# Performance work log

Hardware: AMD Instinct MI355X
Metric: run time of the kernel (lower is better)

The kernel has to match this reference:

```python
import jax, jax.numpy as jnp
import numpy as np

DIM = 1024
STATE = 64
HEADS = 8
EXPAND = 2
INNER = DIM * EXPAND          # 2048
HEAD_DIM = INNER // HEADS     # 256
KERNEL = 4
B, L = 2, 2048
EPS = 1e-5


def setup_inputs() -> dict:
    key = jax.random.key(0)
    ks = jax.random.split(key, 12)
    s = 0.02
    return {
        "input_tensor": jax.random.normal(ks[0], (B, L, DIM), jnp.float32),
        "Wx": jax.random.normal(ks[1], (INNER, DIM), jnp.float32) * s,
        "Wz": jax.random.normal(ks[2], (INNER, DIM), jnp.float32) * s,
        "conv_w": jax.random.normal(ks[3], (INNER, 1, KERNEL), jnp.float32) * s,
        "conv_b": jnp.zeros((INNER,), jnp.float32),
        "Wb": jax.random.normal(ks[4], (HEADS * STATE, INNER), jnp.float32) * s,
        "Wc": jax.random.normal(ks[5], (HEADS * STATE, INNER), jnp.float32) * s,
        "Wdt": jax.random.normal(ks[6], (HEADS, INNER), jnp.float32) * s,
        "b_dt": jnp.zeros((HEADS,), jnp.float32),
        "log_a": jnp.log(jnp.full((HEADS,), 0.5, jnp.float32)),
        "d_param": jnp.ones((HEADS,), jnp.float32),
        "gn_w": jnp.ones((INNER,), jnp.float32),
        "gn_b": jnp.zeros((INNER,), jnp.float32),
        "Wout": jax.random.normal(ks[7], (DIM, INNER), jnp.float32) * s,
    }


def _causal_conv(x, conv_w, conv_b):
    # x: (B, L, INNER); depthwise conv, kernel 4, left-pad 3 (causal)
    x_pad = jnp.pad(x, ((0, 0), (KERNEL - 1, 0), (0, 0)))
    w = conv_w[:, 0, :]  # (INNER, K)
    y = sum(x_pad[:, k:k + x.shape[1], :] * w[:, k] for k in range(KERNEL))
    return y + conv_b


def _ssd_scan(x, b, c, dt, a):
    # x: (B,L,H,P) b,c: (B,L,H,N) dt: (B,L,H) a: (H,)
    state0 = jnp.zeros((x.shape[0], HEADS, STATE, HEAD_DIM), x.dtype)

    def step(state, inp):
        x_t, b_t, c_t, dt_t = inp  # (B,H,P),(B,H,N),(B,H,N),(B,H)
        decay = jnp.exp(dt_t * a)[..., None, None]          # (B,H,1,1)
        b_bar = (dt_t[..., None] * b_t)                      # (B,H,N)
        state = decay * state + b_bar[..., None] * x_t[:, :, None, :]
        y_t = jnp.einsum("bhn,bhnp->bhp", c_t, state)
        return state, y_t

    xs = (x.transpose(1, 0, 2, 3), b.transpose(1, 0, 2, 3),
          c.transpose(1, 0, 2, 3), dt.transpose(1, 0, 2))
    _, ys = jax.lax.scan(step, state0, xs)  # ys: (L,B,H,P)
    return ys.transpose(1, 0, 2, 3)


def reference(input_tensor, Wx, Wz, conv_w, conv_b, Wb, Wc, Wdt, b_dt,
              log_a, d_param, gn_w, gn_b, Wout):
    bsz, seq, _ = input_tensor.shape
    x = input_tensor @ Wx.T               # (B,L,INNER)
    z = input_tensor @ Wz.T
    x = _causal_conv(x, conv_w, conv_b)
    x = jax.nn.silu(x)
    b = (x @ Wb.T).reshape(bsz, seq, HEADS, STATE)
    c = (x @ Wc.T).reshape(bsz, seq, HEADS, STATE)
    dt = jax.nn.softplus(x @ Wdt.T + b_dt)  # (B,L,H)
    xh = x.reshape(bsz, seq, HEADS, HEAD_DIM)
    a = -jnp.exp(log_a)
    y = _ssd_scan(xh, b, c, dt, a)
    y = y + d_param[None, None, :, None] * xh
    # GroupNorm(HEADS, INNER) applied on (B, C, L): normalize per (batch, group)
    # over (channels-in-group, sequence)
    yg = y  # (B, L, H, P) -- groups are contiguous channel blocks = heads
    mean = yg.mean(axis=(1, 3), keepdims=True)
    var = yg.var(axis=(1, 3), keepdims=True)
    yn = (yg - mean) / jnp.sqrt(var + EPS)
    yn = yn * gn_w.reshape(1, 1, HEADS, HEAD_DIM) + gn_b.reshape(1, 1, HEADS, HEAD_DIM)
    yn = yn.reshape(bsz, seq, INNER)
    out = yn * jax.nn.silu(z)
    return out @ Wout.T
```

## Files before the change

### kernel.cpp

```cpp
#include <hip/hip_runtime.h>
#include <math.h>

#define DIM_   1024
#define STATE_ 64
#define HEADS_ 8
#define INNER_ 2048
#define HDIM_  256
#define B_     2
#define L_     2048
#define M_     (B_*L_)
#define EPS_   1e-5f
#define Q_     64
#define NC_    (L_/Q_)
#define NCHUNK_ (B_*HEADS_*NC_)
#define BCS_   1024
#define XZS_   4096

typedef _Float16 f16;
typedef __attribute__((ext_vector_type(8))) _Float16 half8;
typedef __attribute__((ext_vector_type(4))) _Float16 half4;
typedef __attribute__((ext_vector_type(4))) float    f32x4;

__device__ __forceinline__ float siluf(float x) { return x / (1.f + expf(-x)); }

__device__ __forceinline__ void gload_lds16(const void* g, void* l) {
    __builtin_amdgcn_global_load_lds((const __attribute__((address_space(1))) void*)g,
                                     (__attribute__((address_space(3))) void*)l, 16, 0, 0);
}

__global__ __launch_bounds__(256) void cast_all(const float* __restrict__ in0,
                                                const float* __restrict__ Wx,
                                                const float* __restrict__ Wz,
                                                const float* __restrict__ Wb,
                                                const float* __restrict__ Wc,
                                                const float* __restrict__ Wout,
                                                f16* __restrict__ input_h,
                                                f16* __restrict__ wxz_h,
                                                f16* __restrict__ wbc_h,
                                                f16* __restrict__ wout_h) {
    int i = blockIdx.x * 256 + threadIdx.x;
    const float* src; f16* dst; int off;
    if      (i < 1048576) { src = in0;  dst = input_h;            off = i; }
    else if (i < 1572864) { src = Wx;   dst = wxz_h;              off = i - 1048576; }
    else if (i < 2097152) { src = Wz;   dst = wxz_h + 2097152;    off = i - 1572864; }
    else if (i < 2359296) { src = Wb;   dst = wbc_h;              off = i - 2097152; }
    else if (i < 2621440) { src = Wc;   dst = wbc_h + 1048576;    off = i - 2359296; }
    else                  { src = Wout; dst = wout_h;             off = i - 2621440; }
    float4 v = *(const float4*)&src[(size_t)off * 4];
    half4 o;
    o[0] = (f16)v.x; o[1] = (f16)v.y; o[2] = (f16)v.z; o[3] = (f16)v.w;
    *(half4*)&dst[(size_t)off * 4] = o;
}

template<int BN, bool OUTF16, bool SILUZ>
__global__ __launch_bounds__(256) void hgemm(const f16* __restrict__ A,
                                             const f16* __restrict__ W,
                                             void* __restrict__ Cout,
                                             int K, int N) {
    constexpr int N_FR = BN / 32;
    constexpr int NITER = (128 + BN) / 64;
    __shared__ f16 sA[128 * 32];
    __shared__ f16 sW[BN * 32];
    const int tid  = threadIdx.x;
    const int wid  = tid >> 6;
    const int lane = tid & 63;

    const int nwg = gridDim.x * gridDim.y;
    const int id0 = blockIdx.y * gridDim.x + blockIdx.x;
    const int cpx = nwg >> 3;
    const int id  = (id0 & 7) * cpx + (id0 >> 3);
    const int gxsh = __ffs(gridDim.x) - 1;
    const int bm = (id >> gxsh) * 128;
    const int bn = (id & (gridDim.x - 1)) * BN;

    const int wr = wid >> 1, wc = wid & 1;
    const int r  = lane & 15, kg = lane >> 4;

    const f16* gsrc[NITER];
    f16* ldst[NITER];
#pragma unroll
    for (int i = 0; i < NITER; ++i) {
        int slot = tid + i * 256;
        if (slot < 512) {
            int row = slot >> 2;
            int kgv = ((slot & 3) ^ ((row >> 1) & 3)) * 8;
            gsrc[i] = A + (size_t)(bm + row) * K + kgv;
        } else {
            int row = (slot - 512) >> 2;
            int kgv = ((slot & 3) ^ ((row >> 1) & 3)) * 8;
            gsrc[i] = W + (size_t)(bn + row) * K + kgv;
        }
        int slot0 = (tid & ~63) + i * 256;
        ldst[i] = (slot0 < 512) ? &sA[slot0 * 8] : &sW[(slot0 - 512) * 8];
    }

    int aoff[4], boff[N_FR];
#pragma unroll
    for (int m = 0; m < 4; ++m) {
        int arow = wr * 64 + m * 16 + r;
        aoff[m] = arow * 32 + ((kg ^ ((arow >> 1) & 3)) << 3);
    }
#pragma unroll
    for (int n = 0; n < N_FR; ++n) {
        int wrow = wc * (BN / 2) + n * 16 + r;
        boff[n] = wrow * 32 + ((kg ^ ((wrow >> 1) & 3)) << 3);
    }

    f32x4 acc[4][N_FR];
#pragma unroll
    for (int m = 0; m < 4; ++m)
#pragma unroll
        for (int n = 0; n < N_FR; ++n) acc[m][n] = (f32x4)0.f;

    for (int k0 = 0; k0 < K; k0 += 32) {
#pragma unroll
        for (int i = 0; i < NITER; ++i) gload_lds16(gsrc[i] + k0, ldst[i]);
        __syncthreads();
        half8 av[4], bv[N_FR];
#pragma unroll
        for (int m = 0; m < 4; ++m) av[m] = *(const half8*)&sA[aoff[m]];
#pragma unroll
        for (int n = 0; n < N_FR; ++n) bv[n] = *(const half8*)&sW[boff[n]];
#pragma unroll
        for (int m = 0; m < 4; ++m)
#pragma unroll
            for (int n = 0; n < N_FR; ++n)
                acc[m][n] = __builtin_amdgcn_mfma_f32_16x16x32_f16(av[m], bv[n], acc[m][n], 0, 0, 0);
        __syncthreads();
    }

#pragma unroll
    for (int m = 0; m < 4; ++m)
#pragma unroll
        for (int n = 0; n < N_FR; ++n) {
            int row0o = bm + wr * 64 + m * 16 + kg * 4;
            int col   = bn + wc * (BN / 2) + n * 16 + r;
#pragma unroll
            for (int j = 0; j < 4; ++j) {
                float v = acc[m][n][j];
                if (SILUZ && col >= INNER_) v = siluf(v);
                if (OUTF16) ((f16*)Cout)[(size_t)(row0o + j) * N + col] = (f16)v;
                else        ((float*)Cout)[(size_t)(row0o + j) * N + col] = v;
            }
        }
}

__global__ __launch_bounds__(256) void conv_silu_dt(const f16* __restrict__ xz,
                                                    const float* __restrict__ cw,
                                                    const float* __restrict__ cb,
                                                    const float* __restrict__ Wdt,
                                                    const float* __restrict__ bdt,
                                                    f16* __restrict__ xc,
                                                    float* __restrict__ dtb) {
    __shared__ float sred[4][HEADS_];
    const int m = blockIdx.x;
    const int tid = threadIdx.x;
    const int c8 = tid * 8;
    const int t = m & (L_ - 1);
    float acc[8];
    float4 wv[8];
#pragma unroll
    for (int j = 0; j < 8; ++j) { acc[j] = cb[c8 + j]; wv[j] = *(const float4*)&cw[(c8 + j) * 4]; }
#pragma unroll
    for (int k = 0; k < 4; ++k) {
        int tt = t - 3 + k;
        if (tt >= 0) {
            half8 xv = *(const half8*)&xz[(size_t)(m - 3 + k) * XZS_ + c8];
#pragma unroll
            for (int j = 0; j < 8; ++j) acc[j] += (float)xv[j] * ((const float*)&wv[j])[k];
        }
    }
    float xf[8];
    half8 o;
#pragma unroll
    for (int j = 0; j < 8; ++j) { xf[j] = siluf(acc[j]); o[j] = (f16)xf[j]; }
    *(half8*)&xc[(size_t)m * INNER_ + c8] = o;

    float p[HEADS_];
#pragma unroll
    for (int h = 0; h < HEADS_; ++h) {
        float4 w0 = *(const float4*)&Wdt[h * INNER_ + c8];
        float4 w1 = *(const float4*)&Wdt[h * INNER_ + c8 + 4];
        p[h] = xf[0]*w0.x + xf[1]*w0.y + xf[2]*w0.z + xf[3]*w0.w
             + xf[4]*w1.x + xf[5]*w1.y + xf[6]*w1.z + xf[7]*w1.w;
    }
#pragma unroll
    for (int h = 0; h < HEADS_; ++h)
#pragma unroll
        for (int off = 32; off > 0; off >>= 1)
            p[h] += __shfl_down(p[h], off, 64);
    if ((tid & 63) == 0) {
#pragma unroll
        for (int h = 0; h < HEADS_; ++h) sred[tid >> 6][h] = p[h];
    }
    __syncthreads();
    if (tid < 32) {
        float v = sred[tid >> 3][tid & 7];
        v += __shfl_down(v, 16, 32);
        v += __shfl_down(v, 8, 32);
        if (tid < 8) {
            float s = v + bdt[tid];
            dtb[(size_t)m * HEADS_ + tid] = (s > 20.f) ? s : log1pf(expf(s));
        }
    }
}

__global__ __launch_bounds__(256) void xpose_k(const f16* __restrict__ xc,
                                               f16* __restrict__ xT,
                                               float* __restrict__ gstat) {
    __shared__ f16 sT[64][72];
    const int blk = blockIdx.x;
    const int bh = blk >> 7;
    const int rem = blk & 127;
    const int tt = rem >> 2;
    const int pt = rem & 3;
    const int b = bh >> 3, h = bh & 7;
    const int tid = threadIdx.x;
    if (blk == 0 && tid < 2 * B_ * HEADS_) gstat[tid] = 0.f;
#pragma unroll
    for (int it = 0; it < 2; ++it) {
        int q = tid + it * 256;
        int tr = q >> 3;
        int p0 = (q & 7) * 8;
        half8 v = *(const half8*)&xc[(size_t)(b * L_ + tt * 64 + tr) * INNER_ + h * HDIM_ + pt * 64 + p0];
        *(half8*)&sT[tr][p0] = v;
    }
    __syncthreads();
#pragma unroll
    for (int it = 0; it < 2; ++it) {
        int q = tid + it * 256;
        int pr = q >> 3;
        int t0 = (q & 7) * 8;
        half8 v;
#pragma unroll
        for (int j = 0; j < 8; ++j) v[j] = sT[t0 + j][pr];
        *(half8*)&xT[((size_t)bh * HDIM_ + pt * 64 + pr) * L_ + tt * 64 + t0] = v;
    }
}

__global__ __launch_bounds__(256) void ssd12(const f16* __restrict__ bc,
                                             const float* __restrict__ dtb,
                                             const float* __restrict__ log_a,
                                             const f16* __restrict__ xT,
                                             f16* __restrict__ pbuf,
                                             f16* __restrict__ sloc,
                                             float* __restrict__ eAbuf,
                                             float* __restrict__ cdecay) {
    __shared__ float sA[Q_], sDt[Q_], sw[Q_];
    __shared__ f16 sB[Q_ * Q_];
    const int tid = threadIdx.x;
    const int chunk = blockIdx.x;
    const int bh = chunk / NC_;
    const int ck = chunk - bh * NC_;
    const int b = bh >> 3, h = bh & 7;
    const int m0 = b * L_ + ck * Q_;

    const int s0 = tid >> 3,        n00 = (tid & 7) * 8;
    const int s1 = (tid + 256) >> 3, n01 = (tid & 7) * 8;
    half8 bv0 = *(const half8*)&bc[(size_t)(m0 + s0) * BCS_ + h * STATE_ + n00];
    half8 bv1 = *(const half8*)&bc[(size_t)(m0 + s1) * BCS_ + h * STATE_ + n01];

    if (tid < 64) {
        float dt = dtb[(size_t)(m0 + tid) * HEADS_ + h];
        float a = -expf(log_a[h]);
        float x = dt * a;
#pragma unroll
        for (int off = 1; off < 64; off <<= 1) {
            float v = __shfl_up(x, off, 64);
            if (tid >= off) x += v;
        }
        float Alast = __shfl(x, 63, 64);
        sA[tid] = x;
        sDt[tid] = dt;
        sw[tid] = expf(Alast - x) * dt;
        eAbuf[(size_t)(m0 + tid) * HEADS_ + h] = expf(x);
        if (tid == 0) cdecay[chunk] = expf(Alast);
    }
    __syncthreads();

    {
        float w0 = sw[s0], w1 = sw[s1];
        half8 o0, o1;
#pragma unroll
        for (int j = 0; j < 8; ++j) { o0[j] = (f16)((float)bv0[j] * w0); o1[j] = (f16)((float)bv1[j] * w1); }
        *(half8*)&sB[s0 * Q_ + (n00 ^ ((s0 & 7) << 3))] = o0;
        *(half8*)&sB[s1 * Q_ + (n01 ^ ((s1 & 7) << 3))] = o1;
    }

    const int w = tid >> 6, lane = tid & 63;
    const int r = lane & 15, kg = lane >> 4;

    {
        const int ft = w;
        const f16* Crow = bc + (size_t)(m0 + ft * 16 + r) * BCS_ + 512 + h * STATE_;
        half8 a0 = *(const half8*)(Crow + kg * 8);
        half8 a1 = *(const half8*)(Crow + 32 + kg * 8);
#pragma unroll
        for (int fs = 0; fs < 4; ++fs) {
            const f16* Brow = bc + (size_t)(m0 + fs * 16 + r) * BCS_ + h * STATE_;
            half8 b0 = *(const half8*)(Brow + kg * 8);
            half8 b1 = *(const half8*)(Brow + 32 + kg * 8);
            f32x4 g = (f32x4)0.f;
            g = __builtin_amdgcn_mfma_f32_16x16x32_f16(a0, b0, g, 0, 0, 0);
            g = __builtin_amdgcn_mfma_f32_16x16x32_f16(a1, b1, g, 0, 0, 0);
            int s = fs * 16 + r;
            float As = sA[s], dts = sDt[s];
#pragma unroll
            for (int j = 0; j < 4; ++j) {
                int t = ft * 16 + kg * 4 + j;
                float val = (t >= s) ? g[j] * expf(sA[t] - As) * dts : 0.f;
                pbuf[((size_t)chunk * Q_ + t) * Q_ + s] = (f16)val;
            }
        }
    }
    __syncthreads();

    f32x4 acc[4][4];
#pragma unroll
    for (int i = 0; i < 4; ++i)
#pragma unroll
        for (int j = 0; j < 4; ++j) acc[i][j] = (f32x4)0.f;

#pragma unroll
    for (int kk = 0; kk < 2; ++kk) {
        half8 a[4], bfr[4];
#pragma unroll
        for (int pf = 0; pf < 4; ++pf) {
            int p = w * 64 + pf * 16 + r;
            a[pf] = *(const half8*)&xT[((size_t)bh * HDIM_ + p) * L_ + ck * Q_ + kk * 32 + kg * 8];
        }
#pragma unroll
        for (int nf = 0; nf < 4; ++nf) {
            int n = nf * 16 + r;
            half8 v;
#pragma unroll
            for (int j = 0; j < 8; ++j) {
                int s = kk * 32 + kg * 8 + j;
                v[j] = sB[s * Q_ + (n ^ (j << 3))];
            }
            bfr[nf] = v;
        }
#pragma unroll
        for (int pf = 0; pf < 4; ++pf)
#pragma unroll
            for (int nf = 0; nf < 4; ++nf)
                acc[pf][nf] = __builtin_amdgcn_mfma_f32_16x16x32_f16(a[pf], bfr[nf], acc[pf][nf], 0, 0, 0);
    }
#pragma unroll
    for (int pf = 0; pf < 4; ++pf)
#pragma unroll
        for (int nf = 0; nf < 4; ++nf) {
            int n = nf * 16 + r;
#pragma unroll
            for (int j = 0; j < 4; ++j) {
                int p = w * 64 + pf * 16 + kg * 4 + j;
                sloc[((size_t)chunk * HDIM_ + p) * STATE_ + n] = (f16)acc[pf][nf][j];
            }
        }
}

__global__ __launch_bounds__(256) void chunk_scan_k(f16* __restrict__ sloc,
                                                    const float* __restrict__ cdecay) {
    int bh = blockIdx.x >> 4;
    int el4 = (((blockIdx.x & 15) * 256 + threadIdx.x) << 2);
    float s0 = 0.f, s1 = 0.f, s2 = 0.f, s3 = 0.f;
    for (int c = 0; c < NC_; ++c) {
        size_t chunk = (size_t)bh * NC_ + c;
        f16* ptr = sloc + chunk * (size_t)(STATE_ * HDIM_) + el4;
        half4 v = *(const half4*)ptr;
        half4 o; o[0] = (f16)s0; o[1] = (f16)s1; o[2] = (f16)s2; o[3] = (f16)s3;
        *(half4*)ptr = o;
        float d = cdecay[chunk];
        s0 = d * s0 + (float)v[0];
        s1 = d * s1 + (float)v[1];
        s2 = d * s2 + (float)v[2];
        s3 = d * s3 + (float)v[3];
    }
}

__global__ __launch_bounds__(256) void ssd_phase3(const f16* __restrict__ bc,
                                                  const f16* __restrict__ pbuf,
                                                  const f16* __restrict__ xT,
                                                  const f16* __restrict__ sloc,
                                                  const f16* __restrict__ xch,
                                                  const float* __restrict__ eAbuf,
                                                  const float* __restrict__ dparam,
                                                  f16* __restrict__ ybuf,
                                                  float* __restrict__ gstats) {
    __shared__ float red[512];
    const int tid = threadIdx.x;
    const int chunk = blockIdx.x;
    const int bh = chunk / NC_;
    const int ck = chunk - bh * NC_;
    const int b = bh >> 3, h = bh & 7;
    const int m0 = b * L_ + ck * Q_;
    const int w = tid >> 6, lane = tid & 63;
    const int r = lane & 15, kg = lane >> 4;

    float eA[4];
#pragma unroll
    for (int ft = 0; ft < 4; ++ft)
        eA[ft] = eAbuf[(size_t)(m0 + ft * 16 + r) * HEADS_ + h];

    f32x4 acc[4][4];
#pragma unroll
    for (int i = 0; i < 4; ++i)
#pragma unroll
        for (int j = 0; j < 4; ++j) acc[i][j] = (f32x4)0.f;

#pragma unroll
    for (int ks = 0; ks < 4; ++ks) {
        half8 a[4], bfr[4];
#pragma unroll
        for (int ft = 0; ft < 4; ++ft) {
            int t = ft * 16 + r;
            if (ks < 2) {
                a[ft] = *(const half8*)&pbuf[((size_t)chunk * Q_ + t) * Q_ + ks * 32 + kg * 8];
            } else {
                half8 c = *(const half8*)&bc[(size_t)(m0 + t) * BCS_ + 512 + h * STATE_ + (ks - 2) * 32 + kg * 8];
                half8 sc;
#pragma unroll
                for (int j = 0; j < 8; ++j) sc[j] = (f16)(eA[ft] * (float)c[j]);
                a[ft] = sc;
            }
        }
#pragma unroll
        for (int pf = 0; pf < 4; ++pf) {
            int p = w * 64 + pf * 16 + r;
            if (ks < 2)
                bfr[pf] = *(const half8*)&xT[((size_t)bh * HDIM_ + p) * L_ + ck * Q_ + ks * 32 + kg * 8];
            else
                bfr[pf] = *(const half8*)&sloc[((size_t)chunk * HDIM_ + p) * STATE_ + (ks - 2) * 32 + kg * 8];
        }
#pragma unroll
        for (int ft = 0; ft < 4; ++ft)
#pragma unroll
            for (int pf = 0; pf < 4; ++pf)
                acc[ft][pf] = __builtin_amdgcn_mfma_f32_16x16x32_f16(a[ft], bfr[pf], acc[ft][pf], 0, 0, 0);
    }

    const float d = dparam[h];
    float lsum = 0.f, lsq = 0.f;
#pragma unroll
    for (int ft = 0; ft < 4; ++ft)
#pragma unroll
        for (int pf = 0; pf < 4; ++pf) {
            int p = w * 64 + pf * 16 + r;
#pragma unroll
            for (int j = 0; j < 4; ++j) {
                int t = ft * 16 + kg * 4 + j;
                size_t off = (size_t)(m0 + t) * INNER_ + h * HDIM_ + p;
                float y = acc[ft][pf][j] + d * (float)xch[off];
                ybuf[off] = (f16)y;
                lsum += y; lsq += y * y;
            }
        }
    __syncthreads();
    red[tid] = lsum; red[256 + tid] = lsq;
    __syncthreads();
    for (int st = 128; st > 0; st >>= 1) {
        if (tid < st) { red[tid] += red[tid + st]; red[256 + tid] += red[256 + tid + st]; }
        __syncthreads();
    }
    if (tid == 0) {
        atomicAdd(&gstats[bh * 2 + 0], red[0]);
        atomicAdd(&gstats[bh * 2 + 1], red[256]);
    }
}

__global__ __launch_bounds__(256) void gn_gate_h(const f16* __restrict__ ybuf,
                                                 const f16* __restrict__ xz,
                                                 const float* __restrict__ gstats,
                                                 const float* __restrict__ gnw,
                                                 const float* __restrict__ gnb,
                                                 f16* __restrict__ g) {
    int idx = blockIdx.x * 256 + threadIdx.x;
    int c8 = (idx & (INNER_/8 - 1)) * 8;
    int m = idx >> 8;
    int bh = (m >> 11) * HEADS_ + (c8 >> 8);
    const float cnt = (float)(L_ * HDIM_);
    float mean = gstats[bh*2] / cnt;
    float var  = gstats[bh*2+1] / cnt - mean*mean;
    float rstd = rsqrtf(var + EPS_);
    size_t off = (size_t)m * INNER_ + c8;
    half8 yv = *(const half8*)&ybuf[off];
    half8 zv = *(const half8*)&xz[(size_t)m * XZS_ + INNER_ + c8];
    float4 w0 = *(const float4*)&gnw[c8], w1 = *(const float4*)&gnw[c8+4];
    float4 b0 = *(const float4*)&gnb[c8], b1 = *(const float4*)&gnb[c8+4];
    float wv[8] = {w0.x, w0.y, w0.z, w0.w, w1.x, w1.y, w1.z, w1.w};
    float bv[8] = {b0.x, b0.y, b0.z, b0.w, b1.x, b1.y, b1.z, b1.w};
    half8 o;
#pragma unroll
    for (int j = 0; j < 8; ++j) {
        float v = ((float)yv[j] - mean) * rstd * wv[j] + bv[j];
        o[j] = (f16)(v * (float)zv[j]);
    }
    *(half8*)&g[off] = o;
}

extern "C" void kernel_launch(void* const* d_in, const int* in_sizes, int n_in,
                              void* d_out, int out_size, void* d_ws, size_t ws_size,
                              hipStream_t stream) {
    const float* input  = (const float*)d_in[0];
    const float* Wx     = (const float*)d_in[1];
    const float* Wz     = (const float*)d_in[2];
    const float* conv_w = (const float*)d_in[3];
    const float* conv_b = (const float*)d_in[4];
    const float* Wb     = (const float*)d_in[5];
    const float* Wc     = (const float*)d_in[6];
    const float* Wdt    = (const float*)d_in[7];
    const float* b_dt   = (const float*)d_in[8];
    const float* log_a  = (const float*)d_in[9];
    const float* d_par  = (const float*)d_in[10];
    const float* gn_w   = (const float*)d_in[11];
    const float* gn_b   = (const float*)d_in[12];
    const float* Wout   = (const float*)d_in[13];
    float* out = (float*)d_out;

    float* ws = (float*)d_ws;
    size_t off = 0;
    auto alloc = [&](size_t nfloats) { float* p = ws + off; off += (nfloats + 63) & ~(size_t)63; return p; };
    f16* input_h = (f16*)alloc((size_t)M_*DIM_/2);
    f16* wxz_h   = (f16*)alloc((size_t)XZS_*DIM_/2);
    f16* wbc_h   = (f16*)alloc((size_t)BCS_*INNER_/2);
    f16* wout_h  = (f16*)alloc((size_t)DIM_*INNER_/2);
    f16* xz_h    = (f16*)alloc((size_t)M_*XZS_/2);
    f16* xconv_h = (f16*)alloc((size_t)M_*INNER_/2);
    f16* xT_h    = (f16*)alloc((size_t)M_*INNER_/2);
    f16* gbuf_h  = (f16*)alloc((size_t)M_*INNER_/2);
    f16* bcmat_h = (f16*)alloc((size_t)M_*BCS_/2);
    f16* pbuf_h  = (f16*)alloc((size_t)NCHUNK_*Q_*Q_/2);
    f16* sloc_h  = (f16*)alloc((size_t)NCHUNK_*STATE_*HDIM_/2);
    f16* ybuf_h  = (f16*)alloc((size_t)M_*INNER_/2);
    float* dtb   = alloc((size_t)M_*HEADS_);
    float* eAb   = alloc((size_t)M_*HEADS_);
    float* cdec  = alloc((size_t)NCHUNK_);
    float* gstat = alloc((size_t)2*B_*HEADS_);

    dim3 blk(256);

    cast_all<<<12288, blk, 0, stream>>>(input, Wx, Wz, Wb, Wc, Wout,
                                        input_h, wxz_h, wbc_h, wout_h);
    hgemm<128,true,true><<<dim3(XZS_/128, M_/128), blk, 0, stream>>>(input_h, wxz_h, xz_h, DIM_, XZS_);
    conv_silu_dt<<<M_, blk, 0, stream>>>(xz_h, conv_w, conv_b, Wdt, b_dt, xconv_h, dtb);
    hgemm<64,true,false><<<dim3(BCS_/64, M_/128), blk, 0, stream>>>(xconv_h, wbc_h, bcmat_h, INNER_, BCS_);
    xpose_k<<<2048, blk, 0, stream>>>(xconv_h, xT_h, gstat);
    ssd12<<<NCHUNK_, blk, 0, stream>>>(bcmat_h, dtb, log_a, xT_h, pbuf_h, sloc_h, eAb, cdec);
    chunk_scan_k<<<256, blk, 0, stream>>>(sloc_h, cdec);
    ssd_phase3<<<NCHUNK_, blk, 0, stream>>>(bcmat_h, pbuf_h, xT_h, sloc_h, xconv_h,
                                            eAb, d_par, ybuf_h, gstat);
    gn_gate_h<<<(M_*(INNER_/8))/256, blk, 0, stream>>>(ybuf_h, xz_h, gstat, gn_w, gn_b, gbuf_h);
    hgemm<64,false,false><<<dim3(DIM_/64, M_/128), blk, 0, stream>>>(gbuf_h, wout_h, out, INNER_, DIM_);
}
```

Baseline: 363.2 us.

## Double GEMM K-tile to 64, drop tile swizzle, fold D skip into diagonal

The shared fp16 GEMM now stages a K-step of 64 per iteration with an 8-way XOR swizzle, which halves the number of barrier pairs per output tile at the cost of twice the LDS footprint. The grouped workgroup-ID remapping for L2 locality is removed in favour of plain block indexing. The D·x skip term is folded into the intra-chunk diagonal of the P matrix in ssd12, so phase 3 no longer re-reads the conv output. Adding d to the diagonal in fp16 may slightly change numerics.

```diff
diff --git a/kernel.cpp b/kernel.cpp
--- a/kernel.cpp
+++ b/kernel.cpp
@@ -58,21 +58,14 @@
                                              void* __restrict__ Cout,
                                              int K, int N) {
     constexpr int N_FR = BN / 32;
-    constexpr int NITER = (128 + BN) / 64;
-    __shared__ f16 sA[128 * 32];
-    __shared__ f16 sW[BN * 32];
+    constexpr int NITER = (128 + BN) / 32;
+    __shared__ f16 sA[128 * 64];
+    __shared__ f16 sW[BN * 64];
     const int tid  = threadIdx.x;
     const int wid  = tid >> 6;
     const int lane = tid & 63;
-
-    const int nwg = gridDim.x * gridDim.y;
-    const int id0 = blockIdx.y * gridDim.x + blockIdx.x;
-    const int cpx = nwg >> 3;
-    const int id  = (id0 & 7) * cpx + (id0 >> 3);
-    const int gxsh = __ffs(gridDim.x) - 1;
-    const int bm = (id >> gxsh) * 128;
-    const int bn = (id & (gridDim.x - 1)) * BN;
-
+    const int bm = blockIdx.y * 128;
+    const int bn = blockIdx.x * BN;
     const int wr = wid >> 1, wc = wid & 1;
     const int r  = lane & 15, kg = lane >> 4;
 
@@ -81,29 +74,29 @@
 #pragma unroll
     for (int i = 0; i < NITER; ++i) {
         int slot = tid + i * 256;
-        if (slot < 512) {
-            int row = slot >> 2;
-            int kgv = ((slot & 3) ^ ((row >> 1) & 3)) * 8;
-            gsrc[i] = A + (size_t)(bm + row) * K + kgv;
+        if (slot < 1024) {
+            int row = slot >> 3;
+            int col = ((slot & 7) ^ (row & 7)) * 8;
+            gsrc[i] = A + (size_t)(bm + row) * K + col;
         } else {
-            int row = (slot - 512) >> 2;
-            int kgv = ((slot & 3) ^ ((row >> 1) & 3)) * 8;
-            gsrc[i] = W + (size_t)(bn + row) * K + kgv;
+            int row = (slot - 1024) >> 3;
+            int col = ((slot & 7) ^ (row & 7)) * 8;
+            gsrc[i] = W + (size_t)(bn + row) * K + col;
         }
         int slot0 = (tid & ~63) + i * 256;
-        ldst[i] = (slot0 < 512) ? &sA[slot0 * 8] : &sW[(slot0 - 512) * 8];
-    }
-
-    int aoff[4], boff[N_FR];
+        ldst[i] = (slot0 < 1024) ? &sA[slot0 * 8] : &sW[(slot0 - 1024) * 8];
+    }
+
+    int abase[4], axor[4], bbase[N_FR], bxor[N_FR];
 #pragma unroll
     for (int m = 0; m < 4; ++m) {
         int arow = wr * 64 + m * 16 + r;
-        aoff[m] = arow * 32 + ((kg ^ ((arow >> 1) & 3)) << 3);
+        abase[m] = arow * 64; axor[m] = arow & 7;
     }
 #pragma unroll
     for (int n = 0; n < N_FR; ++n) {
         int wrow = wc * (BN / 2) + n * 16 + r;
-        boff[n] = wrow * 32 + ((kg ^ ((wrow >> 1) & 3)) << 3);
+        bbase[n] = wrow * 64; bxor[n] = wrow & 7;
     }
 
     f32x4 acc[4][N_FR];
@@ -112,20 +105,25 @@
 #pragma unroll
         for (int n = 0; n < N_FR; ++n) acc[m][n] = (f32x4)0.f;
 
-    for (int k0 = 0; k0 < K; k0 += 32) {
+    for (int k0 = 0; k0 < K; k0 += 64) {
 #pragma unroll
         for (int i = 0; i < NITER; ++i) gload_lds16(gsrc[i] + k0, ldst[i]);
         __syncthreads();
-        half8 av[4], bv[N_FR];
-#pragma unroll
-        for (int m = 0; m < 4; ++m) av[m] = *(const half8*)&sA[aoff[m]];
-#pragma unroll
-        for (int n = 0; n < N_FR; ++n) bv[n] = *(const half8*)&sW[boff[n]];
-#pragma unroll
-        for (int m = 0; m < 4; ++m)
+#pragma unroll
+        for (int kk = 0; kk < 2; ++kk) {
+            half8 av[4], bv[N_FR];
+#pragma unroll
+            for (int m = 0; m < 4; ++m)
+                av[m] = *(const half8*)&sA[abase[m] + ((((kk << 2) | kg)) ^ axor[m]) * 8];
 #pragma unroll
             for (int n = 0; n < N_FR; ++n)
-                acc[m][n] = __builtin_amdgcn_mfma_f32_16x16x32_f16(av[m], bv[n], acc[m][n], 0, 0, 0);
+                bv[n] = *(const half8*)&sW[bbase[n] + ((((kk << 2) | kg)) ^ bxor[n]) * 8];
+#pragma unroll
+            for (int m = 0; m < 4; ++m)
+#pragma unroll
+                for (int n = 0; n < N_FR; ++n)
+                    acc[m][n] = __builtin_amdgcn_mfma_f32_16x16x32_f16(av[m], bv[n], acc[m][n], 0, 0, 0);
+        }
         __syncthreads();
     }
 
@@ -241,6 +239,7 @@
 __global__ __launch_bounds__(256) void ssd12(const f16* __restrict__ bc,
                                              const float* __restrict__ dtb,
                                              const float* __restrict__ log_a,
+                                             const float* __restrict__ dparam,
                                              const f16* __restrict__ xT,
                                              f16* __restrict__ pbuf,
                                              f16* __restrict__ sloc,
@@ -291,6 +290,7 @@
     const int r = lane & 15, kg = lane >> 4;
 
     {
+        const float dpar = dparam[h];
         const int ft = w;
         const f16* Crow = bc + (size_t)(m0 + ft * 16 + r) * BCS_ + 512 + h * STATE_;
         half8 a0 = *(const half8*)(Crow + kg * 8);
@@ -309,6 +309,7 @@
             for (int j = 0; j < 4; ++j) {
                 int t = ft * 16 + kg * 4 + j;
                 float val = (t >= s) ? g[j] * expf(sA[t] - As) * dts : 0.f;
+                if (t == s) val += dpar;
                 pbuf[((size_t)chunk * Q_ + t) * Q_ + s] = (f16)val;
             }
         }
@@ -382,11 +383,10 @@
                                                   const f16* __restrict__ pbuf,
                                                   const f16* __restrict__ xT,
                                                   const f16* __restrict__ sloc,
-                                                  const f16* __restrict__ xch,
                                                   const float* __restrict__ eAbuf,
-                                                  const float* __restrict__ dparam,
-                                                  f16* __restrict__ ybuf,
+                                                  float* __restrict__ ybuf16_,
                                                   float* __restrict__ gstats) {
+    f16* ybuf = (f16*)ybuf16_;
     __shared__ float red[512];
     const int tid = threadIdx.x;
     const int chunk = blockIdx.x;
@@ -439,7 +439,6 @@
                 acc[ft][pf] = __builtin_amdgcn_mfma_f32_16x16x32_f16(a[ft], bfr[pf], acc[ft][pf], 0, 0, 0);
     }
 
-    const float d = dparam[h];
     float lsum = 0.f, lsq = 0.f;
 #pragma unroll
     for (int ft = 0; ft < 4; ++ft)
@@ -450,7 +449,7 @@
             for (int j = 0; j < 4; ++j) {
                 int t = ft * 16 + kg * 4 + j;
                 size_t off = (size_t)(m0 + t) * INNER_ + h * HDIM_ + p;
-                float y = acc[ft][pf][j] + d * (float)xch[off];
+                float y = acc[ft][pf][j];
                 ybuf[off] = (f16)y;
                 lsum += y; lsq += y * y;
             }
@@ -545,10 +544,10 @@
     conv_silu_dt<<<M_, blk, 0, stream>>>(xz_h, conv_w, conv_b, Wdt, b_dt, xconv_h, dtb);
     hgemm<64,true,false><<<dim3(BCS_/64, M_/128), blk, 0, stream>>>(xconv_h, wbc_h, bcmat_h, INNER_, BCS_);
     xpose_k<<<2048, blk, 0, stream>>>(xconv_h, xT_h, gstat);
-    ssd12<<<NCHUNK_, blk, 0, stream>>>(bcmat_h, dtb, log_a, xT_h, pbuf_h, sloc_h, eAb, cdec);
+    ssd12<<<NCHUNK_, blk, 0, stream>>>(bcmat_h, dtb, log_a, d_par, xT_h, pbuf_h, sloc_h, eAb, cdec);
     chunk_scan_k<<<256, blk, 0, stream>>>(sloc_h, cdec);
-    ssd_phase3<<<NCHUNK_, blk, 0, stream>>>(bcmat_h, pbuf_h, xT_h, sloc_h, xconv_h,
-                                            eAb, d_par, ybuf_h, gstat);
+    ssd_phase3<<<NCHUNK_, blk, 0, stream>>>(bcmat_h, pbuf_h, xT_h, sloc_h,
+                                            eAb, (float*)ybuf_h, gstat);
     gn_gate_h<<<(M_*(INNER_/8))/256, blk, 0, stream>>>(ybuf_h, xz_h, gstat, gn_w, gn_b, gbuf_h);
     hgemm<64,false,false><<<dim3(DIM_/64, M_/128), blk, 0, stream>>>(gbuf_h, wout_h, out, INNER_, DIM_);
 }
```

After: 349.0 us. -3.9%, faster.
